# Kernel optimization log

Measured on AMD Instinct MI355X. Metric: run time of the kernel, lower is better.

Reference implementation:

```python
import jax, jax.numpy as jnp
import numpy as np

U, I, N, E, F, H, TOPK = 2048, 16384, 18432, 1_000_000, 64, 32, 3
NEG = -1e30  # stands in for 'structural zero' entries excluded from top-k


def setup_inputs() -> dict:
    key = jax.random.key(0)
    ks = jax.random.split(key, 6)
    x = jax.random.normal(ks[0], (N, F), dtype=jnp.float32)
    w1 = jax.random.normal(ks[1], (H, 2 * F + 2), dtype=jnp.float32) * 0.1
    b1 = jnp.zeros((H,), dtype=jnp.float32)
    w2 = jax.random.normal(ks[2], (1, H), dtype=jnp.float32) * 0.1
    b2 = jnp.zeros((1,), dtype=jnp.float32)
    edge_src = jax.random.randint(ks[3], (E,), 0, U)        # user-local == global (user_idx = arange)
    edge_dst_item = jax.random.randint(ks[4], (E,), 0, I)   # item-local; global item id = U + item
    user_idx = jnp.arange(U, dtype=jnp.int64) if jax.config.jax_enable_x64 else jnp.arange(U, dtype=jnp.int32)
    return {"x": x, "w1": w1, "b1": b1, "w2": w2, "b2": b2,
            "edge_src": edge_src, "edge_dst_item": edge_dst_item,
            "user_idx": user_idx, "num_nodes": N}


def reference(x, w1, b1, w2, b2, edge_src, edge_dst_item, user_idx, num_nodes):
    num_users = user_idx.shape[0]
    num_items = num_nodes - num_users
    u_local = edge_src           # user_idx = arange(U) so user_map is identity
    i_local = edge_dst_item      # item nodes occupy indices [U, N)

    ones = jnp.ones(u_local.shape[0], dtype=jnp.float32)
    d_u = jnp.log1p(jax.ops.segment_sum(ones, u_local, num_segments=num_users))  # [U]
    d_i = jnp.log1p(jax.ops.segment_sum(ones, i_local, num_segments=num_items))  # [I]

    # per-edge features: [u_x, log1p(deg_u), i_x, log1p(deg_i)] -> [E, 2F+2]
    x_u = x[user_idx[u_local]]
    x_it = x[num_users + i_local]
    x_e = jnp.concatenate([x_u, d_u[u_local][:, None], x_it, d_i[i_local][:, None]], axis=1)
    h = jax.nn.relu(x_e @ w1.T + b1)
    w = jax.nn.sigmoid(h @ w2.T + b2)[:, 0]  # [E], edge weights in (0,1)

    # A' [U, I] (duplicate edges coalesce-summed), C = A' A'^T with degree scaling
    A = jnp.zeros((num_users, num_items), dtype=jnp.float32).at[u_local, i_local].add(w)
    C = A @ A.T
    Dh = jnp.sqrt(d_u)
    C = C * Dh[:, None] * Dh[None, :]

    # per-row top-k restricted to structural nonzeros (all weights > 0)
    Cm = jnp.where(C > 0, C, NEG)
    vals, idx = jax.lax.top_k(Cm, TOPK)          # [U, K]
    valid = vals > 0
    vhalf = jnp.where(valid, vals, 0.0) * 0.5
    rows = jnp.broadcast_to(jnp.arange(num_users)[:, None], (num_users, TOPK))
    T = jnp.zeros((num_users, num_users), dtype=jnp.float32).at[rows, idx].add(vhalf)
    S = T + T.T  # symmetrized, deduped-by-sum adjacency; S[r,c] = val of edge (r,c)
    return S, d_u
```

## Files before the change

kernel.cpp:

```cpp
#include <hip/hip_runtime.h>
#include <hip/hip_bf16.h>
#include <math.h>

#define U_N 2048
#define I_N 16384
#define F_N 64
#define H_N 32
#define KDIM 16384
#define NEGV (-1e30f)
#define NB_DEG 128

typedef __attribute__((ext_vector_type(8))) short short8;
typedef __attribute__((ext_vector_type(4))) float f32x4;

__device__ __forceinline__ unsigned short f2bf(float f) {
    unsigned int u = __builtin_bit_cast(unsigned int, f);
    return (unsigned short)((u + 0x7fffu + ((u >> 16) & 1u)) >> 16);
}

__device__ __forceinline__ void gload16(const void* g, void* l) {
    __builtin_amdgcn_global_load_lds(
        (const __attribute__((address_space(1))) unsigned int*)g,
        (__attribute__((address_space(3))) unsigned int*)l, 16, 0, 0);
}

__global__ __launch_bounds__(256) void k_deg_part(const int* __restrict__ src,
                                                  const int* __restrict__ dst, int E,
                                                  unsigned int* __restrict__ pu,
                                                  unsigned int* __restrict__ pi2) {
    __shared__ unsigned int hu[U_N];
    __shared__ unsigned int hi2[I_N / 2];
    int tid = threadIdx.x;
    for (int t = tid; t < U_N; t += 256) hu[t] = 0u;
    for (int t = tid; t < I_N / 2; t += 256) hi2[t] = 0u;
    __syncthreads();
    for (int e = blockIdx.x * 256 + tid; e < E; e += NB_DEG * 256) {
        int u = src[e], i = dst[e];
        atomicAdd(&hu[u], 1u);
        atomicAdd(&hi2[i >> 1], 1u << ((i & 1) * 16));
    }
    __syncthreads();
    unsigned int* pub = pu + (size_t)blockIdx.x * U_N;
    unsigned int* pib = pi2 + (size_t)blockIdx.x * (I_N / 2);
    for (int t = tid; t < U_N; t += 256) pub[t] = hu[t];
    for (int t = tid; t < I_N / 2; t += 256) pib[t] = hi2[t];
}

__global__ __launch_bounds__(256) void k_node(const unsigned int* __restrict__ pu,
                                              const unsigned int* __restrict__ pi2,
                                              float* __restrict__ du,
                                              float* __restrict__ di,
                                              float* __restrict__ Dh,
                                              float* __restrict__ out_du,
                                              unsigned int* __restrict__ degu) {
    int t = blockIdx.x * 256 + threadIdx.x;
    if (t < U_N) {
        unsigned int s = 0;
        for (int b = 0; b < NB_DEG; ++b) s += pu[(size_t)b * U_N + t];
        degu[t] = s;
        float v = log1pf((float)s);
        du[t] = v;
        Dh[t] = sqrtf(v);
        out_du[t] = v;
    }
    if (t < I_N / 2) {
        unsigned int s = 0;
        for (int b = 0; b < NB_DEG; ++b) s += pi2[(size_t)b * (I_N / 2) + t];
        di[2 * t]     = log1pf((float)(s & 0xffffu));
        di[2 * t + 1] = log1pf((float)(s >> 16));
    }
}

__global__ __launch_bounds__(256) void k_scan2(const unsigned int* __restrict__ pu,
                                               const unsigned int* __restrict__ degu,
                                               unsigned int* __restrict__ base,
                                               unsigned int* __restrict__ pof) {
    __shared__ unsigned int s[U_N];
    __shared__ unsigned int csum[256];
    int tid = threadIdx.x;
    for (int t = tid; t < U_N; t += 256) s[t] = degu[t];
    __syncthreads();
    unsigned int sum = 0;
#pragma unroll
    for (int j = 0; j < 8; ++j) sum += s[tid * 8 + j];
    csum[tid] = sum;
    __syncthreads();
    if (tid == 0) {
        unsigned int run = 0;
        for (int c = 0; c < 256; ++c) { unsigned int v = csum[c]; csum[c] = run; run += v; }
    }
    __syncthreads();
    {
        unsigned int run = csum[tid];
        unsigned int ex[8];
#pragma unroll
        for (int j = 0; j < 8; ++j) { ex[j] = run; run += s[tid * 8 + j]; }
        __syncthreads();
#pragma unroll
        for (int j = 0; j < 8; ++j) s[tid * 8 + j] = ex[j];
        __syncthreads();
    }
    int u = blockIdx.x * 256 + tid;
    unsigned int run = s[u];
    base[u] = run;
    for (int b = 0; b < NB_DEG; ++b) {
        pof[(size_t)b * U_N + u] = run;
        run += pu[(size_t)b * U_N + u];
    }
}

__global__ __launch_bounds__(256) void k_esort(const int* __restrict__ src,
                                               const int* __restrict__ dst, int E,
                                               const unsigned int* __restrict__ pof,
                                               int* __restrict__ sorted) {
    __shared__ unsigned int cur[U_N];
    int tid = threadIdx.x;
    const unsigned int* p = pof + (size_t)blockIdx.x * U_N;
    for (int t = tid; t < U_N; t += 256) cur[t] = p[t];
    __syncthreads();
    for (int e = blockIdx.x * 256 + tid; e < E; e += NB_DEG * 256) {
        int u = src[e];
        unsigned int slot = atomicAdd(&cur[u], 1u);
        sorted[slot] = dst[e];
    }
}

__global__ __launch_bounds__(256) void k_proj(const float* __restrict__ x,
                                              const float* __restrict__ w1,
                                              const float* __restrict__ b1,
                                              const float* __restrict__ du,
                                              const float* __restrict__ di,
                                              float* __restrict__ Pu,
                                              float* __restrict__ Pi) {
    int t = blockIdx.x * 256 + threadIdx.x;
    if (t < U_N * H_N) {
        int u = t >> 5, j = t & 31;
        const float* xr = x + (size_t)u * F_N;
        const float* wr = w1 + (size_t)j * (2 * F_N + 2);
        float acc = b1[j] + du[u] * wr[64];
#pragma unroll
        for (int f = 0; f < F_N; ++f) acc = fmaf(xr[f], wr[f], acc);
        Pu[t] = acc;
    } else if (t < U_N * H_N + I_N * H_N) {
        int t2 = t - U_N * H_N;
        int i = t2 >> 5, j = t2 & 31;
        const float* xr = x + (size_t)(U_N + i) * F_N;
        const float* wr = w1 + (size_t)j * (2 * F_N + 2) + 65;
        float acc = di[i] * wr[64];
#pragma unroll
        for (int f = 0; f < F_N; ++f) acc = fmaf(xr[f], wr[f], acc);
        Pi[t2] = acc;
    }
}

__global__ __launch_bounds__(256) void k_edge2(const int* __restrict__ sorted,
                                               const unsigned int* __restrict__ base,
                                               const unsigned int* __restrict__ degu,
                                               const float* __restrict__ Pu,
                                               const float* __restrict__ Pi,
                                               const float* __restrict__ w2,
                                               const float* __restrict__ b2,
                                               unsigned int* __restrict__ Aw,
                                               float* __restrict__ diag) {
    __shared__ float hrow[I_N];
    __shared__ float red[256];
    int u = blockIdx.x, tid = threadIdx.x;
    for (int t = tid; t < I_N; t += 256) hrow[t] = 0.f;

    float pur[H_N], w2r[H_N];
#pragma unroll
    for (int j = 0; j < H_N; ++j) pur[j] = Pu[(size_t)u * H_N + j];
#pragma unroll
    for (int j = 0; j < H_N; ++j) w2r[j] = w2[j];
    float bb = b2[0];
    __syncthreads();

    int nb = (int)base[u], d = (int)degu[u];
    for (int k = tid; k < d; k += 256) {
        int i = sorted[nb + k];
        const float4* pi4 = (const float4*)(Pi + (size_t)i * H_N);
        float acc = bb;
#pragma unroll
        for (int q = 0; q < H_N / 4; ++q) {
            float4 b = pi4[q];
            acc = fmaf(fmaxf(pur[4 * q + 0] + b.x, 0.f), w2r[4 * q + 0], acc);
            acc = fmaf(fmaxf(pur[4 * q + 1] + b.y, 0.f), w2r[4 * q + 1], acc);
            acc = fmaf(fmaxf(pur[4 * q + 2] + b.z, 0.f), w2r[4 * q + 2], acc);
            acc = fmaf(fmaxf(pur[4 * q + 3] + b.w, 0.f), w2r[4 * q + 3], acc);
        }
        float wgt = 1.0f / (1.0f + expf(-acc));
        atomicAdd(&hrow[i], wgt);
    }
    __syncthreads();

    unsigned int* row = Aw + (size_t)u * (I_N / 2);
    float ss = 0.f;
    for (int w = tid; w < I_N / 2; w += 256) {
        float lo = hrow[2 * w], hi = hrow[2 * w + 1];
        row[w] = (unsigned int)f2bf(lo) | ((unsigned int)f2bf(hi) << 16);
        ss = fmaf(lo, lo, ss);
        ss = fmaf(hi, hi, ss);
    }
    red[tid] = ss;
    __syncthreads();
#pragma unroll
    for (int s = 128; s > 0; s >>= 1) {
        if (tid < s) red[tid] += red[tid + s];
        __syncthreads();
    }
    if (tid == 0) diag[u] = red[0];
}

#define BM 128
#define BKS 64
#define NBLK (U_N / BM)
#define NPAIR (NBLK * (NBLK + 1) / 2)
#define KSPLIT 8
#define KCH (KDIM / KSPLIT)

__global__ __launch_bounds__(256) void k_syrk(const unsigned short* __restrict__ Abf,
                                              float* __restrict__ C) {
    __shared__ unsigned short As[BM * BKS];
    __shared__ unsigned short Bs[BM * BKS];

    int k0 = blockIdx.x * KCH;
    int p = blockIdx.y;
    int bi = 0, rem = p;
    while (rem >= NBLK - bi) { rem -= NBLK - bi; ++bi; }
    int bj = bi + rem;
    int diagp = (bi == bj);

    int tid = threadIdx.x;
    int wave = tid >> 6, lane = tid & 63;

    int srow = wave * 32 + (lane >> 3);
    int scol = ((lane & 7) ^ (lane >> 3)) * 8;
    const unsigned short* Ag = Abf + (size_t)(bi * BM + srow) * KDIM + k0 + scol;
    const unsigned short* Bg = Abf + (size_t)(bj * BM + srow) * KDIM + k0 + scol;
    unsigned short* lA = As + (wave * 32) * BKS;
    unsigned short* lB = Bs + (wave * 32) * BKS;

    int wm = wave >> 1, wn = wave & 1;
    int lm = lane & 15, lq = lane >> 4;
    int lm7 = lm & 7;
    const unsigned short* bTile = diagp ? As : Bs;

    f32x4 acc[4][4];
#pragma unroll
    for (int m = 0; m < 4; ++m)
#pragma unroll
        for (int n = 0; n < 4; ++n) acc[m][n] = (f32x4){0.f, 0.f, 0.f, 0.f};

    for (int kt = 0; kt < KCH; kt += BKS) {
        __syncthreads();
#pragma unroll
        for (int j = 0; j < 4; ++j)
            gload16(Ag + kt + (size_t)(j * 8) * KDIM, lA + j * 8 * BKS);
        if (!diagp) {
#pragma unroll
            for (int j = 0; j < 4; ++j)
                gload16(Bg + kt + (size_t)(j * 8) * KDIM, lB + j * 8 * BKS);
        }
        __syncthreads();

#pragma unroll
        for (int s = 0; s < 2; ++s) {
            int pos = ((lq + s * 4) ^ lm7) * 8;
            short8 av[4], bv[4];
#pragma unroll
            for (int m = 0; m < 4; ++m)
                av[m] = *(const short8*)(As + (wm * 64 + m * 16 + lm) * BKS + pos);
#pragma unroll
            for (int n = 0; n < 4; ++n)
                bv[n] = *(const short8*)(bTile + (wn * 64 + n * 16 + lm) * BKS + pos);
#pragma unroll
            for (int m = 0; m < 4; ++m)
#pragma unroll
                for (int n = 0; n < 4; ++n)
                    acc[m][n] = __builtin_amdgcn_mfma_f32_16x16x32_bf16(
                        av[m], bv[n], acc[m][n], 0, 0, 0);
        }
    }

#pragma unroll
    for (int m = 0; m < 4; ++m) {
        int rb = bi * BM + wm * 64 + m * 16 + lq * 4;
#pragma unroll
        for (int n = 0; n < 4; ++n) {
            int c = bj * BM + wn * 64 + n * 16 + lm;
            f32x4 v = acc[m][n];
#pragma unroll
            for (int g = 0; g < 4; ++g)
                atomicAdd(&C[(size_t)(rb + g) * U_N + c], v[g]);
        }
    }
}

__global__ __launch_bounds__(256) void k_mirror(float* __restrict__ C) {
    __shared__ float T[64][65];
    int tr = blockIdx.x, tc = blockIdx.y;
    if ((tr >> 1) <= (tc >> 1)) return;
    int lane = threadIdx.x & 63;
    int w = threadIdx.x >> 6;
#pragma unroll
    for (int s = 0; s < 16; ++s) {
        int r = s * 4 + w;
        T[r][lane] = C[(size_t)(tc * 64 + r) * U_N + tr * 64 + lane];
    }
    __syncthreads();
#pragma unroll
    for (int s = 0; s < 16; ++s) {
        int r = s * 4 + w;
        C[(size_t)(tr * 64 + r) * U_N + tc * 64 + lane] = T[lane][r];
    }
}

__device__ __forceinline__ bool better(float va, int ia, float vb, int ib) {
    return (va > vb) || (va == vb && ia < ib);
}
__device__ __forceinline__ void ins3(float v, int i, float& v0, int& i0,
                                     float& v1, int& i1, float& v2, int& i2) {
    if (better(v, i, v0, i0)) { v2 = v1; i2 = i1; v1 = v0; i1 = i0; v0 = v; i0 = i; }
    else if (better(v, i, v1, i1)) { v2 = v1; i2 = i1; v1 = v; i1 = i; }
    else if (better(v, i, v2, i2)) { v2 = v; i2 = i; }
}

__global__ __launch_bounds__(64) void k_topk(const float* __restrict__ C,
                                             const float* __restrict__ Dh,
                                             const float* __restrict__ diag,
                                             float* __restrict__ topv,
                                             int* __restrict__ topi) {
    int r = blockIdx.x;
    int lane = threadIdx.x;
    float dr = Dh[r];
    float dex = diag[r] * dr * dr;
    float dval = (dex > 0.f) ? dex : NEGV;
    const float4* row = (const float4*)(C + (size_t)r * U_N);
    const float4* dh4 = (const float4*)Dh;
    float v0 = NEGV, v1 = NEGV, v2 = NEGV;
    int i0 = 0x7fffffff, i1 = 0x7fffffff, i2 = 0x7fffffff;
    int qr = r >> 2;
    for (int q = lane; q < U_N / 4; q += 64) {
        float4 cv = row[q];
        float4 dv = dh4[q];
        int c = q * 4;
        float x0 = (cv.x > 0.f) ? cv.x * dr * dv.x : NEGV;
        float x1 = (cv.y > 0.f) ? cv.y * dr * dv.y : NEGV;
        float x2 = (cv.z > 0.f) ? cv.z * dr * dv.z : NEGV;
        float x3 = (cv.w > 0.f) ? cv.w * dr * dv.w : NEGV;
        if (q == qr) {
            int j = r & 3;
            if (j == 0) x0 = dval; else if (j == 1) x1 = dval;
            else if (j == 2) x2 = dval; else x3 = dval;
        }
        if (better(x0, c + 0, v2, i2)) ins3(x0, c + 0, v0, i0, v1, i1, v2, i2);
        if (better(x1, c + 1, v2, i2)) ins3(x1, c + 1, v0, i0, v1, i1, v2, i2);
        if (better(x2, c + 2, v2, i2)) ins3(x2, c + 2, v0, i0, v1, i1, v2, i2);
        if (better(x3, c + 3, v2, i2)) ins3(x3, c + 3, v0, i0, v1, i1, v2, i2);
    }
#pragma unroll
    for (int off = 1; off < 64; off <<= 1) {
        float ov0 = __shfl_xor(v0, off), ov1 = __shfl_xor(v1, off), ov2 = __shfl_xor(v2, off);
        int oi0 = __shfl_xor(i0, off), oi1 = __shfl_xor(i1, off), oi2 = __shfl_xor(i2, off);
        ins3(ov0, oi0, v0, i0, v1, i1, v2, i2);
        ins3(ov1, oi1, v0, i0, v1, i1, v2, i2);
        ins3(ov2, oi2, v0, i0, v1, i1, v2, i2);
    }
    if (lane == 0) {
        topv[r * 3 + 0] = v0; topi[r * 3 + 0] = i0;
        topv[r * 3 + 1] = v1; topi[r * 3 + 1] = i1;
        topv[r * 3 + 2] = v2; topi[r * 3 + 2] = i2;
    }
}

__global__ __launch_bounds__(256) void k_scatter(const float* __restrict__ topv,
                                                 const int* __restrict__ topi,
                                                 float* __restrict__ out) {
    int r = blockIdx.x * 256 + threadIdx.x;
    if (r >= U_N) return;
#pragma unroll
    for (int k = 0; k < 3; ++k) {
        float v = topv[r * 3 + k];
        int c = topi[r * 3 + k];
        if (v > 0.f) {
            atomicAdd(&out[(size_t)r * U_N + c], 0.5f * v);
            atomicAdd(&out[(size_t)c * U_N + r], 0.5f * v);
        }
    }
}

extern "C" void kernel_launch(void* const* d_in, const int* in_sizes, int n_in,
                              void* d_out, int out_size, void* d_ws, size_t ws_size,
                              hipStream_t stream) {
    const float* x  = (const float*)d_in[0];
    const float* w1 = (const float*)d_in[1];
    const float* b1 = (const float*)d_in[2];
    const float* w2 = (const float*)d_in[3];
    const float* b2 = (const float*)d_in[4];
    const int* esrc = (const int*)d_in[5];
    const int* edst = (const int*)d_in[6];
    int E = in_sizes[5];
    float* out = (float*)d_out;

    unsigned short* Abf = (unsigned short*)d_ws;
    float* C    = (float*)(Abf + (size_t)U_N * I_N);
    float* Pu   = C + (size_t)U_N * U_N;
    float* Pi   = Pu + (size_t)U_N * H_N;
    unsigned int* pu  = (unsigned int*)(Pi + (size_t)I_N * H_N);
    unsigned int* pi2 = pu + (size_t)NB_DEG * U_N;
    unsigned int* pof = pi2 + (size_t)NB_DEG * (I_N / 2);
    unsigned int* degu = pof + (size_t)NB_DEG * U_N;
    unsigned int* base = degu + U_N;
    float* du   = (float*)(base + U_N);
    float* di   = du + U_N;
    float* Dh   = di + I_N;
    float* diag = Dh + U_N;
    float* topv = diag + U_N;
    int*   topi = (int*)(topv + U_N * 3);
    int*   sorted = topi + U_N * 3;

    hipMemsetAsync(C, 0, (size_t)U_N * U_N * sizeof(float), stream);
    hipMemsetAsync(out, 0, (size_t)out_size * sizeof(float), stream);

    k_deg_part<<<NB_DEG, 256, 0, stream>>>(esrc, edst, E, pu, pi2);
    k_node<<<(I_N / 2 + 255) / 256, 256, 0, stream>>>(pu, pi2, du, di, Dh,
                                                      out + (size_t)U_N * U_N, degu);
    k_scan2<<<U_N / 256, 256, 0, stream>>>(pu, degu, base, pof);
    k_proj<<<(U_N * H_N + I_N * H_N) / 256, 256, 0, stream>>>(x, w1, b1, du, di, Pu, Pi);
    k_esort<<<NB_DEG, 256, 0, stream>>>(esrc, edst, E, pof, sorted);
    k_edge2<<<U_N, 256, 0, stream>>>(sorted, base, degu, Pu, Pi, w2, b2,
                                     (unsigned int*)Abf, diag);
    k_syrk<<<dim3(KSPLIT, NPAIR), 256, 0, stream>>>(Abf, C);
    k_mirror<<<dim3(U_N / 64, U_N / 64), 256, 0, stream>>>(C);
    k_topk<<<U_N, 64, 0, stream>>>(C, Dh, diag, topv, topi);
    k_scatter<<<(U_N + 255) / 256, 256, 0, stream>>>(topv, topi, out);
}
```

Measured before the change: 348.5 us.

## Vectorize edge passes, shrink sorted indices, fuse scatter into top-k, retune splits

Edge histogram and sort passes now read src/dst as int4, with more partial-histogram blocks. Sorted item ids are stored as 16-bit values to halve that buffer's traffic. The edge kernel zeroes and packs its row with 128-bit accesses. The top-k kernel runs four rows per block and does the output scatter itself, which removes a kernel launch and the intermediate top-k buffers. The SYRK K-split is halved and the scan kernel is reshaped to 64 threads, so the prefix pass over partials now does more serial work per thread.

```diff
diff --git a/kernel.cpp b/kernel.cpp
--- a/kernel.cpp
+++ b/kernel.cpp
@@ -8,7 +8,7 @@
 #define H_N 32
 #define KDIM 16384
 #define NEGV (-1e30f)
-#define NB_DEG 128
+#define NB_DEG 256
 
 typedef __attribute__((ext_vector_type(8))) short short8;
 typedef __attribute__((ext_vector_type(4))) float f32x4;
@@ -34,10 +34,23 @@
     for (int t = tid; t < U_N; t += 256) hu[t] = 0u;
     for (int t = tid; t < I_N / 2; t += 256) hi2[t] = 0u;
     __syncthreads();
-    for (int e = blockIdx.x * 256 + tid; e < E; e += NB_DEG * 256) {
-        int u = src[e], i = dst[e];
-        atomicAdd(&hu[u], 1u);
-        atomicAdd(&hi2[i >> 1], 1u << ((i & 1) * 16));
+    const int4* s4 = (const int4*)src;
+    const int4* d4 = (const int4*)dst;
+    int nv = E >> 2;
+    for (int v = blockIdx.x * 256 + tid; v < nv; v += NB_DEG * 256) {
+        int4 u = s4[v], i = d4[v];
+        atomicAdd(&hu[u.x], 1u); atomicAdd(&hi2[i.x >> 1], 1u << ((i.x & 1) * 16));
+        atomicAdd(&hu[u.y], 1u); atomicAdd(&hi2[i.y >> 1], 1u << ((i.y & 1) * 16));
+        atomicAdd(&hu[u.z], 1u); atomicAdd(&hi2[i.z >> 1], 1u << ((i.z & 1) * 16));
+        atomicAdd(&hu[u.w], 1u); atomicAdd(&hi2[i.w >> 1], 1u << ((i.w & 1) * 16));
+    }
+    if (blockIdx.x == 0) {
+        int e = nv * 4 + tid;
+        if (e < E) {
+            atomicAdd(&hu[src[e]], 1u);
+            int i = dst[e];
+            atomicAdd(&hi2[i >> 1], 1u << ((i & 1) * 16));
+        }
     }
     __syncthreads();
     unsigned int* pub = pu + (size_t)blockIdx.x * U_N;
@@ -71,36 +84,36 @@
     }
 }
 
-__global__ __launch_bounds__(256) void k_scan2(const unsigned int* __restrict__ pu,
-                                               const unsigned int* __restrict__ degu,
-                                               unsigned int* __restrict__ base,
-                                               unsigned int* __restrict__ pof) {
+__global__ __launch_bounds__(64) void k_scan2(const unsigned int* __restrict__ pu,
+                                              const unsigned int* __restrict__ degu,
+                                              unsigned int* __restrict__ base,
+                                              unsigned int* __restrict__ pof) {
     __shared__ unsigned int s[U_N];
-    __shared__ unsigned int csum[256];
+    __shared__ unsigned int csum[64];
     int tid = threadIdx.x;
-    for (int t = tid; t < U_N; t += 256) s[t] = degu[t];
+    for (int t = tid; t < U_N; t += 64) s[t] = degu[t];
     __syncthreads();
     unsigned int sum = 0;
 #pragma unroll
-    for (int j = 0; j < 8; ++j) sum += s[tid * 8 + j];
+    for (int j = 0; j < 32; ++j) sum += s[tid * 32 + j];
     csum[tid] = sum;
     __syncthreads();
     if (tid == 0) {
         unsigned int run = 0;
-        for (int c = 0; c < 256; ++c) { unsigned int v = csum[c]; csum[c] = run; run += v; }
+        for (int c = 0; c < 64; ++c) { unsigned int v = csum[c]; csum[c] = run; run += v; }
     }
     __syncthreads();
     {
         unsigned int run = csum[tid];
-        unsigned int ex[8];
-#pragma unroll
-        for (int j = 0; j < 8; ++j) { ex[j] = run; run += s[tid * 8 + j]; }
+        unsigned int ex[32];
+#pragma unroll
+        for (int j = 0; j < 32; ++j) { ex[j] = run; run += s[tid * 32 + j]; }
         __syncthreads();
 #pragma unroll
-        for (int j = 0; j < 8; ++j) s[tid * 8 + j] = ex[j];
+        for (int j = 0; j < 32; ++j) s[tid * 32 + j] = ex[j];
         __syncthreads();
     }
-    int u = blockIdx.x * 256 + tid;
+    int u = blockIdx.x * 64 + tid;
     unsigned int run = s[u];
     base[u] = run;
     for (int b = 0; b < NB_DEG; ++b) {
@@ -112,16 +125,26 @@
 __global__ __launch_bounds__(256) void k_esort(const int* __restrict__ src,
                                                const int* __restrict__ dst, int E,
                                                const unsigned int* __restrict__ pof,
-                                               int* __restrict__ sorted) {
+                                               unsigned short* __restrict__ sorted) {
     __shared__ unsigned int cur[U_N];
     int tid = threadIdx.x;
     const unsigned int* p = pof + (size_t)blockIdx.x * U_N;
     for (int t = tid; t < U_N; t += 256) cur[t] = p[t];
     __syncthreads();
-    for (int e = blockIdx.x * 256 + tid; e < E; e += NB_DEG * 256) {
-        int u = src[e];
-        unsigned int slot = atomicAdd(&cur[u], 1u);
-        sorted[slot] = dst[e];
+    const int4* s4 = (const int4*)src;
+    const int4* d4 = (const int4*)dst;
+    int nv = E >> 2;
+    for (int v = blockIdx.x * 256 + tid; v < nv; v += NB_DEG * 256) {
+        int4 u = s4[v], i = d4[v];
+        sorted[atomicAdd(&cur[u.x], 1u)] = (unsigned short)i.x;
+        sorted[atomicAdd(&cur[u.y], 1u)] = (unsigned short)i.y;
+        sorted[atomicAdd(&cur[u.z], 1u)] = (unsigned short)i.z;
+        sorted[atomicAdd(&cur[u.w], 1u)] = (unsigned short)i.w;
+    }
+    if (blockIdx.x == 0) {
+        int e = nv * 4 + tid;
+        if (e < E)
+            sorted[atomicAdd(&cur[src[e]], 1u)] = (unsigned short)dst[e];
     }
 }
 
@@ -153,19 +176,22 @@
     }
 }
 
-__global__ __launch_bounds__(256) void k_edge2(const int* __restrict__ sorted,
+__global__ __launch_bounds__(256) void k_edge2(const unsigned short* __restrict__ sorted,
                                                const unsigned int* __restrict__ base,
                                                const unsigned int* __restrict__ degu,
                                                const float* __restrict__ Pu,
                                                const float* __restrict__ Pi,
                                                const float* __restrict__ w2,
                                                const float* __restrict__ b2,
-                                               unsigned int* __restrict__ Aw,
+                                               uint4* __restrict__ Aw,
                                                float* __restrict__ diag) {
     __shared__ float hrow[I_N];
     __shared__ float red[256];
     int u = blockIdx.x, tid = threadIdx.x;
-    for (int t = tid; t < I_N; t += 256) hrow[t] = 0.f;
+    float4* h4 = (float4*)hrow;
+    float4 z4 = {0.f, 0.f, 0.f, 0.f};
+#pragma unroll
+    for (int j = 0; j < 16; ++j) h4[tid + j * 256] = z4;
 
     float pur[H_N], w2r[H_N];
 #pragma unroll
@@ -177,7 +203,7 @@
 
     int nb = (int)base[u], d = (int)degu[u];
     for (int k = tid; k < d; k += 256) {
-        int i = sorted[nb + k];
+        int i = (int)sorted[nb + k];
         const float4* pi4 = (const float4*)(Pi + (size_t)i * H_N);
         float acc = bb;
 #pragma unroll
@@ -193,13 +219,22 @@
     }
     __syncthreads();
 
-    unsigned int* row = Aw + (size_t)u * (I_N / 2);
+    uint4* row = Aw + (size_t)u * (I_N / 8);
     float ss = 0.f;
-    for (int w = tid; w < I_N / 2; w += 256) {
-        float lo = hrow[2 * w], hi = hrow[2 * w + 1];
-        row[w] = (unsigned int)f2bf(lo) | ((unsigned int)f2bf(hi) << 16);
-        ss = fmaf(lo, lo, ss);
-        ss = fmaf(hi, hi, ss);
+#pragma unroll
+    for (int j = 0; j < 8; ++j) {
+        int w = tid + j * 256;
+        float4 a = h4[2 * w], b = h4[2 * w + 1];
+        uint4 o;
+        o.x = (unsigned int)f2bf(a.x) | ((unsigned int)f2bf(a.y) << 16);
+        o.y = (unsigned int)f2bf(a.z) | ((unsigned int)f2bf(a.w) << 16);
+        o.z = (unsigned int)f2bf(b.x) | ((unsigned int)f2bf(b.y) << 16);
+        o.w = (unsigned int)f2bf(b.z) | ((unsigned int)f2bf(b.w) << 16);
+        row[w] = o;
+        ss = fmaf(a.x, a.x, ss); ss = fmaf(a.y, a.y, ss);
+        ss = fmaf(a.z, a.z, ss); ss = fmaf(a.w, a.w, ss);
+        ss = fmaf(b.x, b.x, ss); ss = fmaf(b.y, b.y, ss);
+        ss = fmaf(b.z, b.z, ss); ss = fmaf(b.w, b.w, ss);
     }
     red[tid] = ss;
     __syncthreads();
@@ -215,7 +250,7 @@
 #define BKS 64
 #define NBLK (U_N / BM)
 #define NPAIR (NBLK * (NBLK + 1) / 2)
-#define KSPLIT 8
+#define KSPLIT 4
 #define KCH (KDIM / KSPLIT)
 
 __global__ __launch_bounds__(256) void k_syrk(const unsigned short* __restrict__ Abf,
@@ -325,13 +360,12 @@
     else if (better(v, i, v2, i2)) { v2 = v; i2 = i; }
 }
 
-__global__ __launch_bounds__(64) void k_topk(const float* __restrict__ C,
-                                             const float* __restrict__ Dh,
-                                             const float* __restrict__ diag,
-                                             float* __restrict__ topv,
-                                             int* __restrict__ topi) {
-    int r = blockIdx.x;
-    int lane = threadIdx.x;
+__global__ __launch_bounds__(256) void k_topk(const float* __restrict__ C,
+                                              const float* __restrict__ Dh,
+                                              const float* __restrict__ diag,
+                                              float* __restrict__ out) {
+    int wave = threadIdx.x >> 6, lane = threadIdx.x & 63;
+    int r = blockIdx.x * 4 + wave;
     float dr = Dh[r];
     float dex = diag[r] * dr * dr;
     float dval = (dex > 0.f) ? dex : NEGV;
@@ -367,24 +401,14 @@
         ins3(ov2, oi2, v0, i0, v1, i1, v2, i2);
     }
     if (lane == 0) {
-        topv[r * 3 + 0] = v0; topi[r * 3 + 0] = i0;
-        topv[r * 3 + 1] = v1; topi[r * 3 + 1] = i1;
-        topv[r * 3 + 2] = v2; topi[r * 3 + 2] = i2;
-    }
-}
-
-__global__ __launch_bounds__(256) void k_scatter(const float* __restrict__ topv,
-                                                 const int* __restrict__ topi,
-                                                 float* __restrict__ out) {
-    int r = blockIdx.x * 256 + threadIdx.x;
-    if (r >= U_N) return;
-#pragma unroll
-    for (int k = 0; k < 3; ++k) {
-        float v = topv[r * 3 + k];
-        int c = topi[r * 3 + k];
-        if (v > 0.f) {
-            atomicAdd(&out[(size_t)r * U_N + c], 0.5f * v);
-            atomicAdd(&out[(size_t)c * U_N + r], 0.5f * v);
+        float vs[3] = {v0, v1, v2};
+        int is[3] = {i0, i1, i2};
+#pragma unroll
+        for (int k = 0; k < 3; ++k) {
+            if (vs[k] > 0.f) {
+                atomicAdd(&out[(size_t)r * U_N + is[k]], 0.5f * vs[k]);
+                atomicAdd(&out[(size_t)is[k] * U_N + r], 0.5f * vs[k]);
+            }
         }
     }
 }
@@ -415,9 +439,7 @@
     float* di   = du + U_N;
     float* Dh   = di + I_N;
     float* diag = Dh + U_N;
-    float* topv = diag + U_N;
-    int*   topi = (int*)(topv + U_N * 3);
-    int*   sorted = topi + U_N * 3;
+    unsigned short* sorted = (unsigned short*)(diag + U_N);
 
     hipMemsetAsync(C, 0, (size_t)U_N * U_N * sizeof(float), stream);
     hipMemsetAsync(out, 0, (size_t)out_size * sizeof(float), stream);
@@ -425,13 +447,12 @@
     k_deg_part<<<NB_DEG, 256, 0, stream>>>(esrc, edst, E, pu, pi2);
     k_node<<<(I_N / 2 + 255) / 256, 256, 0, stream>>>(pu, pi2, du, di, Dh,
                                                       out + (size_t)U_N * U_N, degu);
-    k_scan2<<<U_N / 256, 256, 0, stream>>>(pu, degu, base, pof);
+    k_scan2<<<U_N / 64, 64, 0, stream>>>(pu, degu, base, pof);
     k_proj<<<(U_N * H_N + I_N * H_N) / 256, 256, 0, stream>>>(x, w1, b1, du, di, Pu, Pi);
     k_esort<<<NB_DEG, 256, 0, stream>>>(esrc, edst, E, pof, sorted);
     k_edge2<<<U_N, 256, 0, stream>>>(sorted, base, degu, Pu, Pi, w2, b2,
-                                     (unsigned int*)Abf, diag);
+                                     (uint4*)Abf, diag);
     k_syrk<<<dim3(KSPLIT, NPAIR), 256, 0, stream>>>(Abf, C);
     k_mirror<<<dim3(U_N / 64, U_N / 64), 256, 0, stream>>>(C);
-    k_topk<<<U_N, 64, 0, stream>>>(C, Dh, diag, topv, topi);
-    k_scatter<<<(U_N + 255) / 256, 256, 0, stream>>>(topv, topi, out);
-}
+    k_topk<<<U_N / 4, 256, 0, stream>>>(C, Dh, diag, out);
+}
```

Result: faster. 334.5 us (-4.0%).
